# Kernel tuning notes

Measured on AMD Instinct MI355X. Metric: run time of the kernel, lower is better.

Reference implementation:

```python
import jax, jax.numpy as jnp
import numpy as np

HEADS = 4
DIM_HEAD = 128
DIM = 512
FMAP = 32
BATCH = 16


def setup_inputs() -> dict:
    key = jax.random.key(0)
    k1, k2, k3, k4 = jax.random.split(key, 4)
    inner = HEADS * DIM_HEAD
    scale = DIM_HEAD ** -0.5
    fmap = jax.random.normal(k1, (BATCH, DIM, FMAP, FMAP), dtype=jnp.float32)
    # 1x1 conv weight, squeezed: [3*inner_dim, dim]
    w_qkv = jax.random.normal(k2, (3 * inner, DIM), dtype=jnp.float32) * (DIM ** -0.5)
    emb_h = jax.random.normal(k3, (FMAP, DIM_HEAD), dtype=jnp.float32) * scale
    emb_w = jax.random.normal(k4, (FMAP, DIM_HEAD), dtype=jnp.float32) * scale
    return {"fmap": fmap, "w_qkv": w_qkv, "emb_h": emb_h, "emb_w": emb_w}


def reference(fmap, w_qkv, emb_h, emb_w):
    b, c, h, w = fmap.shape
    n = h * w
    scale = DIM_HEAD ** -0.5
    # 1x1 conv == channel matmul: [b, 3*inner, h, w]
    qkv = jnp.einsum('bchw,oc->bohw', fmap, w_qkv)
    # split and rearrange 'b (hd d) x y -> b hd (x y) d'
    qkv = qkv.reshape(b, 3, HEADS, DIM_HEAD, n)          # b 3 H d n
    qkv = jnp.transpose(qkv, (1, 0, 2, 4, 3))            # 3 b H n d
    q, k, v = qkv[0], qkv[1], qkv[2]
    q = q * scale
    # content logits
    sim = jnp.einsum('bhid,bhjd->bhij', q, k)
    # absolute position bias: emb[(x,y)] = emb_h[x] + emb_w[y]
    emb = (emb_h[:, None, :] + emb_w[None, :, :]).reshape(n, DIM_HEAD)
    sim = sim + jnp.einsum('bhid,jd->bhij', q, emb)
    attn = jax.nn.softmax(sim, axis=-1)
    out = jnp.einsum('bhij,bhjd->bhid', attn, v)         # b H n d
    # 'b h (x y) d -> b (h d) x y'
    out = jnp.transpose(out, (0, 1, 3, 2)).reshape(b, HEADS * DIM_HEAD, h, w)
    return out
```

## Files before the change

kernel.cpp:

```cpp
#include <hip/hip_runtime.h>

#define HEADS 4
#define DHEAD 128
#define DIM   512
#define NTOK  1024
#define BATCH 16
#define OCH   1536

typedef unsigned short u16;
typedef short bf16x8 __attribute__((ext_vector_type(8)));
typedef float f32x4  __attribute__((ext_vector_type(4)));

struct alignas(8) us4 { u16 x, y, z, w; };

static __device__ __forceinline__ u16 f2bf(float f) {
    unsigned int u = __float_as_uint(f);
    u = (u + 0x7FFFu + ((u >> 16) & 1u)) >> 16;
    return (u16)u;
}
static __device__ __forceinline__ float bf2f(u16 h) {
    return __uint_as_float(((unsigned int)h) << 16);
}

__global__ __launch_bounds__(256)
void prep_ft(const float* __restrict__ F, u16* __restrict__ fthi, u16* __restrict__ ftlo)
{
    __shared__ float T[32][33];
    const int n0 = blockIdx.x * 32;
    const int c0 = blockIdx.y * 32;
    const int b  = blockIdx.z;
    const int tid = threadIdx.x;

    {
        const int c  = tid >> 3;
        const int n4 = (tid & 7) * 4;
        const float4 f4 = *(const float4*)(&F[((size_t)b * DIM + c0 + c) * NTOK + n0 + n4]);
        T[c][n4 + 0] = f4.x; T[c][n4 + 1] = f4.y; T[c][n4 + 2] = f4.z; T[c][n4 + 3] = f4.w;
    }
    __syncthreads();
    {
        const int n  = tid >> 3;
        const int c4 = (tid & 7) * 4;
        us4 H, L;
        float v0 = T[c4 + 0][n], v1 = T[c4 + 1][n], v2 = T[c4 + 2][n], v3 = T[c4 + 3][n];
        H.x = f2bf(v0); L.x = f2bf(v0 - bf2f(H.x));
        H.y = f2bf(v1); L.y = f2bf(v1 - bf2f(H.y));
        H.z = f2bf(v2); L.z = f2bf(v2 - bf2f(H.z));
        H.w = f2bf(v3); L.w = f2bf(v3 - bf2f(H.w));
        const size_t o = ((size_t)b * NTOK + n0 + n) * DIM + c0 + c4;
        *(us4*)&fthi[o] = H;
        *(us4*)&ftlo[o] = L;
    }
}

__global__ __launch_bounds__(256)
void prep_w(const float* __restrict__ W, u16* __restrict__ wbhi, u16* __restrict__ wblo)
{
    const size_t idx = ((size_t)blockIdx.x * 256 + threadIdx.x) * 8;
    const float4 a = *(const float4*)(&W[idx]);
    const float4 b = *(const float4*)(&W[idx + 4]);
    float v[8] = {a.x, a.y, a.z, a.w, b.x, b.y, b.z, b.w};
    u16 H[8], L[8];
#pragma unroll
    for (int j = 0; j < 8; ++j) {
        H[j] = f2bf(v[j]);
        L[j] = f2bf(v[j] - bf2f(H[j]));
    }
    *(bf16x8*)&wbhi[idx] = *(bf16x8*)H;
    *(bf16x8*)&wblo[idx] = *(bf16x8*)L;
}

__global__ __launch_bounds__(256)
void qkv_mfma(const u16* __restrict__ fthi, const u16* __restrict__ ftlo,
              const u16* __restrict__ wbhi, const u16* __restrict__ wblo,
              const float* __restrict__ EH, const float* __restrict__ EW,
              u16* __restrict__ qhi, u16* __restrict__ qlo,
              u16* __restrict__ khi, u16* __restrict__ klo,
              u16* __restrict__ vtg)
{
    __shared__ u16 smem[16384];
    u16* Ah = smem;
    u16* Al = smem + 4096;
    u16* Bh = smem + 8192;
    u16* Bl = smem + 12288;
    float* Od = (float*)smem;

    const int tid  = threadIdx.x;
    const int lane = tid & 63;
    const int wave = tid >> 6;
    const int l15  = lane & 15;
    const int lg   = lane >> 4;
    const int wm   = wave >> 1;
    const int wn   = wave & 1;

    const int ii = blockIdx.x * 64;
    const int oo = blockIdx.y * 64;
    const int b  = blockIdx.z;
    const size_t fbase = (size_t)b * NTOK * DIM;

    f32x4 acc[2][2];
#pragma unroll
    for (int mf = 0; mf < 2; ++mf)
#pragma unroll
        for (int nf = 0; nf < 2; ++nf) { acc[mf][nf][0] = 0.f; acc[mf][nf][1] = 0.f; acc[mf][nf][2] = 0.f; acc[mf][nf][3] = 0.f; }

    for (int kt = 0; kt < DIM; kt += 64) {
        __syncthreads();
#pragma unroll
        for (int u = 0; u < 2; ++u) {
            const int idx = tid + 256 * u;
            const int j  = idx >> 3;
            const int dc = (idx & 7) * 8;
            const int ld = j * 64 + (dc ^ ((j & 7) << 3));
            const size_t ga = fbase + (size_t)(ii + j) * DIM + kt + dc;
            const size_t gb = (size_t)(oo + j) * DIM + kt + dc;
            *(bf16x8*)&Ah[ld] = *(const bf16x8*)(fthi + ga);
            *(bf16x8*)&Al[ld] = *(const bf16x8*)(ftlo + ga);
            *(bf16x8*)&Bh[ld] = *(const bf16x8*)(wbhi + gb);
            *(bf16x8*)&Bl[ld] = *(const bf16x8*)(wblo + gb);
        }
        __syncthreads();

#pragma unroll
        for (int kc = 0; kc < 2; ++kc) {
            const int ko = kc * 32 + lg * 8;
            bf16x8 af_h[2], af_l[2], bf_h[2], bf_l[2];
#pragma unroll
            for (int mf = 0; mf < 2; ++mf) {
                const int ar = wm * 32 + mf * 16 + l15;
                const int off = ar * 64 + (ko ^ ((ar & 7) << 3));
                af_h[mf] = *(const bf16x8*)&Ah[off];
                af_l[mf] = *(const bf16x8*)&Al[off];
            }
#pragma unroll
            for (int nf = 0; nf < 2; ++nf) {
                const int br = wn * 32 + nf * 16 + l15;
                const int off = br * 64 + (ko ^ ((br & 7) << 3));
                bf_h[nf] = *(const bf16x8*)&Bh[off];
                bf_l[nf] = *(const bf16x8*)&Bl[off];
            }
#pragma unroll
            for (int mf = 0; mf < 2; ++mf)
#pragma unroll
                for (int nf = 0; nf < 2; ++nf) {
                    acc[mf][nf] = __builtin_amdgcn_mfma_f32_16x16x32_bf16(af_h[mf], bf_h[nf], acc[mf][nf], 0, 0, 0);
                    acc[mf][nf] = __builtin_amdgcn_mfma_f32_16x16x32_bf16(af_h[mf], bf_l[nf], acc[mf][nf], 0, 0, 0);
                    acc[mf][nf] = __builtin_amdgcn_mfma_f32_16x16x32_bf16(af_l[mf], bf_h[nf], acc[mf][nf], 0, 0, 0);
                }
        }
    }

    __syncthreads();
#pragma unroll
    for (int mf = 0; mf < 2; ++mf)
#pragma unroll
        for (int nf = 0; nf < 2; ++nf)
#pragma unroll
            for (int r = 0; r < 4; ++r)
                Od[(wm * 32 + mf * 16 + lg * 4 + r) * 68 + wn * 32 + nf * 16 + l15] = acc[mf][nf][r];
    __syncthreads();

    const int s  = oo >> 9;
    const int h  = (oo >> 7) & 3;
    const int d0 = oo & 127;
    const int bh = b * HEADS + h;
    const float scale = 0.08838834764831845f;

    if (s == 2) {
#pragma unroll
        for (int u = 0; u < 2; ++u) {
            const int idx = tid + 256 * u;
            const int dr = idx >> 3;
            const int tc = (idx & 7) * 8;
            u16 P[8];
#pragma unroll
            for (int j = 0; j < 8; ++j)
                P[j] = f2bf(Od[(tc + j) * 68 + dr]);
            *(bf16x8*)&vtg[((size_t)bh * DHEAD + d0 + dr) * NTOK + ii + tc] = *(bf16x8*)P;
        }
    } else {
        u16* hi = s ? khi : qhi;
        u16* lo = s ? klo : qlo;
#pragma unroll
        for (int u = 0; u < 2; ++u) {
            const int idx = tid + 256 * u;
            const int tr = idx >> 3;
            const int dc = (idx & 7) * 8;
            const int i  = ii + tr;
            float v[8];
            const float4 p0 = *(const float4*)&Od[tr * 68 + dc];
            const float4 p1 = *(const float4*)&Od[tr * 68 + dc + 4];
            v[0] = p0.x; v[1] = p0.y; v[2] = p0.z; v[3] = p0.w;
            v[4] = p1.x; v[5] = p1.y; v[6] = p1.z; v[7] = p1.w;
            if (s == 0) {
#pragma unroll
                for (int j = 0; j < 8; ++j) v[j] *= scale;
            } else {
                const float* eh = &EH[(i >> 5) * DHEAD + d0 + dc];
                const float* ew = &EW[(i & 31) * DHEAD + d0 + dc];
                const float4 e0 = *(const float4*)eh, e1 = *(const float4*)(eh + 4);
                const float4 w0 = *(const float4*)ew, w1 = *(const float4*)(ew + 4);
                v[0] += e0.x + w0.x; v[1] += e0.y + w0.y; v[2] += e0.z + w0.z; v[3] += e0.w + w0.w;
                v[4] += e1.x + w1.x; v[5] += e1.y + w1.y; v[6] += e1.z + w1.z; v[7] += e1.w + w1.w;
            }
            u16 H[8], L[8];
#pragma unroll
            for (int j = 0; j < 8; ++j) {
                H[j] = f2bf(v[j]);
                L[j] = f2bf(v[j] - bf2f(H[j]));
            }
            const size_t o = ((size_t)bh * NTOK + i) * DHEAD + d0 + dc;
            *(bf16x8*)&hi[o] = *(bf16x8*)H;
            *(bf16x8*)&lo[o] = *(bf16x8*)L;
        }
    }
}

#define QB 64
#define KB 64

__global__ __launch_bounds__(256, 2)
void attn_mfma(const u16* __restrict__ qh, const u16* __restrict__ ql,
               const u16* __restrict__ kh, const u16* __restrict__ kl,
               const u16* __restrict__ vtg, float* __restrict__ out)
{
    __shared__ u16 smem[28672];
    u16* Kh = smem;
    u16* Kl = smem + 8192;
    u16* Vt = smem + 16384;
    u16* Pl = smem + 24576;
    float* Od = (float*)smem;

    const int tid  = threadIdx.x;
    const int lane = tid & 63;
    const int wave = tid >> 6;
    const int l15  = lane & 15;
    const int lg   = lane >> 4;

    const int ii = blockIdx.x * QB;
    const int bh = blockIdx.y;
    const size_t base = (size_t)bh * NTOK * DHEAD;

    bf16x8 qfh[4], qfl[4];
    {
        const size_t qoff = base + (size_t)(ii + wave * 16 + l15) * DHEAD + lg * 8;
#pragma unroll
        for (int kc = 0; kc < 4; ++kc) {
            qfh[kc] = *(const bf16x8*)(qh + qoff + kc * 32);
            qfl[kc] = *(const bf16x8*)(ql + qoff + kc * 32);
        }
    }

    f32x4 o[8];
#pragma unroll
    for (int n = 0; n < 8; ++n) { o[n][0] = 0.f; o[n][1] = 0.f; o[n][2] = 0.f; o[n][3] = 0.f; }
    float mrow[4], lrow[4];
#pragma unroll
    for (int r = 0; r < 4; ++r) { mrow[r] = -3.0e38f; lrow[r] = 0.f; }

    for (int jt = 0; jt < NTOK / KB; ++jt) {
        __syncthreads();
#pragma unroll
        for (int u = 0; u < 4; ++u) {
            const int idx = tid + 256 * u;
            const int j  = idx >> 4;
            const int dc = (idx & 15) * 8;
            const size_t g = base + (size_t)(jt * KB + j) * DHEAD + dc;
            const int ld = j * DHEAD + (dc ^ ((j & 7) << 3));
            *(bf16x8*)&Kh[ld] = *(const bf16x8*)(kh + g);
            *(bf16x8*)&Kl[ld] = *(const bf16x8*)(kl + g);
        }
#pragma unroll
        for (int u = 0; u < 4; ++u) {
            const int idx = tid + 256 * u;
            const int d  = idx >> 3;
            const int jc = (idx & 7) * 8;
            const size_t g = base + (size_t)d * NTOK + jt * KB + jc;
            *(bf16x8*)&Vt[d * KB + (jc ^ ((d & 7) << 3))] = *(const bf16x8*)(vtg + g);
        }
        __syncthreads();

        f32x4 s[4];
#pragma unroll
        for (int n = 0; n < 4; ++n) {
            f32x4 acc = {0.f, 0.f, 0.f, 0.f};
            const int j  = n * 16 + l15;
            const int ro = j * DHEAD;
            const int sw = (j & 7) << 3;
#pragma unroll
            for (int kc = 0; kc < 4; ++kc) {
                const int off = ro + ((kc * 32 + lg * 8) ^ sw);
                const bf16x8 kb = *(const bf16x8*)&Kh[off];
                const bf16x8 lb = *(const bf16x8*)&Kl[off];
                acc = __builtin_amdgcn_mfma_f32_16x16x32_bf16(qfh[kc], kb, acc, 0, 0, 0);
                acc = __builtin_amdgcn_mfma_f32_16x16x32_bf16(qfh[kc], lb, acc, 0, 0, 0);
                acc = __builtin_amdgcn_mfma_f32_16x16x32_bf16(qfl[kc], kb, acc, 0, 0, 0);
            }
            s[n] = acc;
        }

        float tmax[4];
#pragma unroll
        for (int r = 0; r < 4; ++r)
            tmax[r] = fmaxf(fmaxf(s[0][r], s[1][r]), fmaxf(s[2][r], s[3][r]));
#pragma unroll
        for (int off = 1; off < 16; off <<= 1)
#pragma unroll
            for (int r = 0; r < 4; ++r)
                tmax[r] = fmaxf(tmax[r], __shfl_xor(tmax[r], off));

        float fr[4], psum[4];
#pragma unroll
        for (int r = 0; r < 4; ++r) {
            const float mn = fmaxf(mrow[r], tmax[r]);
            fr[r] = __expf(mrow[r] - mn);
            mrow[r] = mn;
            psum[r] = 0.f;
        }
        const int pbase = wave * 1024;
#pragma unroll
        for (int n = 0; n < 4; ++n)
#pragma unroll
            for (int r = 0; r < 4; ++r) {
                const float p = __expf(s[n][r] - mrow[r]);
                psum[r] += p;
                const int row = lg * 4 + r;
                Pl[pbase + row * KB + ((n * 16 + l15) ^ ((row & 7) << 3))] = f2bf(p);
            }
#pragma unroll
        for (int off = 1; off < 16; off <<= 1)
#pragma unroll
            for (int r = 0; r < 4; ++r)
                psum[r] += __shfl_xor(psum[r], off);
#pragma unroll
        for (int r = 0; r < 4; ++r) lrow[r] = lrow[r] * fr[r] + psum[r];
#pragma unroll
        for (int n = 0; n < 8; ++n)
#pragma unroll
            for (int r = 0; r < 4; ++r) o[n][r] *= fr[r];

        const bf16x8 pf0 = *(const bf16x8*)&Pl[pbase + l15 * KB + ((lg * 8) ^ ((l15 & 7) << 3))];
        const bf16x8 pf1 = *(const bf16x8*)&Pl[pbase + l15 * KB + ((32 + lg * 8) ^ ((l15 & 7) << 3))];
#pragma unroll
        for (int nd = 0; nd < 8; ++nd) {
            const int d  = nd * 16 + l15;
            const int vo = d * KB;
            const int sw = (d & 7) << 3;
            o[nd] = __builtin_amdgcn_mfma_f32_16x16x32_bf16(
                        pf0, *(const bf16x8*)&Vt[vo + ((lg * 8) ^ sw)], o[nd], 0, 0, 0);
            o[nd] = __builtin_amdgcn_mfma_f32_16x16x32_bf16(
                        pf1, *(const bf16x8*)&Vt[vo + ((32 + lg * 8) ^ sw)], o[nd], 0, 0, 0);
        }
    }

    __syncthreads();
    float invl[4];
#pragma unroll
    for (int r = 0; r < 4; ++r) invl[r] = 1.0f / lrow[r];
#pragma unroll
    for (int nd = 0; nd < 8; ++nd)
#pragma unroll
        for (int r = 0; r < 4; ++r)
            Od[(nd * 16 + l15) * 72 + wave * 16 + lg * 4 + r] = o[nd][r] * invl[r];
    __syncthreads();

    const int b = bh >> 2, h = bh & 3;
    float* dst = out + ((size_t)b * 512 + h * DHEAD) * NTOK + ii;
#pragma unroll
    for (int u = 0; u < 4; ++u) {
        const int idx = tid + 256 * u;
        const int d  = idx >> 3;
        const int jc = (idx & 7) * 8;
        *(float4*)(dst + (size_t)d * NTOK + jc)     = *(const float4*)&Od[d * 72 + jc];
        *(float4*)(dst + (size_t)d * NTOK + jc + 4) = *(const float4*)&Od[d * 72 + jc + 4];
    }
}

extern "C" void kernel_launch(void* const* d_in, const int* in_sizes, int n_in,
                              void* d_out, int out_size, void* d_ws, size_t ws_size,
                              hipStream_t stream)
{
    (void)in_sizes; (void)n_in; (void)out_size; (void)ws_size;
    const float* fmap  = (const float*)d_in[0];
    const float* w_qkv = (const float*)d_in[1];
    const float* eh    = (const float*)d_in[2];
    const float* ew    = (const float*)d_in[3];
    float* out = (float*)d_out;

    const size_t per = (size_t)BATCH * HEADS * NTOK * DHEAD;
    u16* qhi  = (u16*)d_ws;
    u16* qlo  = qhi + per;
    u16* khi  = qlo + per;
    u16* klo  = khi + per;
    u16* vtg  = klo + per;
    u16* fthi = vtg + per;
    u16* ftlo = fthi + per;
    u16* wbhi = ftlo + per;
    u16* wblo = wbhi + (size_t)OCH * DIM;

    hipLaunchKernelGGL(prep_ft, dim3(NTOK / 32, DIM / 32, BATCH), dim3(256), 0, stream,
                       fmap, fthi, ftlo);
    hipLaunchKernelGGL(prep_w, dim3((OCH * DIM) / (256 * 8)), dim3(256), 0, stream,
                       w_qkv, wbhi, wblo);
    hipLaunchKernelGGL(qkv_mfma, dim3(NTOK / 64, OCH / 64, BATCH), dim3(256), 0, stream,
                       fthi, ftlo, wbhi, wblo, eh, ew, qhi, qlo, khi, klo, vtg);
    hipLaunchKernelGGL(attn_mfma, dim3(NTOK / QB, BATCH * HEADS), dim3(256), 0, stream,
                       qhi, qlo, khi, klo, vtg, out);
}
```

Baseline: 307.3 us.

## Prefetch next K/V and GEMM tiles into registers during MFMA compute

In both the QKV projection GEMM and the attention kernel, the global loads for the next tile are issued into registers before the current tile's MFMA work and written to shared memory after it. This hides global memory latency behind compute without adding a second LDS buffer. The attention kernel also raises wave priority around its MFMA sections with s_setprio, and the QKV kernel gains a min-2-blocks launch bound. The cost is more live registers per thread, which can cut occupancy or cause spills.

Result: no change. 301.4 us (-1.9%).

```diff
diff --git a/kernel.cpp b/kernel.cpp
--- a/kernel.cpp
+++ b/kernel.cpp
@@ -70,7 +70,7 @@
     *(bf16x8*)&wblo[idx] = *(bf16x8*)L;
 }
 
-__global__ __launch_bounds__(256)
+__global__ __launch_bounds__(256, 2)
 void qkv_mfma(const u16* __restrict__ fthi, const u16* __restrict__ ftlo,
               const u16* __restrict__ wbhi, const u16* __restrict__ wblo,
               const float* __restrict__ EH, const float* __restrict__ EW,
@@ -98,28 +98,45 @@
     const int b  = blockIdx.z;
     const size_t fbase = (size_t)b * NTOK * DIM;
 
+    const int jrow = tid >> 3;
+    const int dc   = (tid & 7) * 8;
+    const int ld0  = jrow * 64 + (dc ^ ((jrow & 7) << 3));
+    const size_t ga0 = fbase + (size_t)(ii + jrow) * DIM + dc;
+    const size_t gb0 = (size_t)(oo + jrow) * DIM + dc;
+
     f32x4 acc[2][2];
 #pragma unroll
     for (int mf = 0; mf < 2; ++mf)
 #pragma unroll
         for (int nf = 0; nf < 2; ++nf) { acc[mf][nf][0] = 0.f; acc[mf][nf][1] = 0.f; acc[mf][nf][2] = 0.f; acc[mf][nf][3] = 0.f; }
 
+    bf16x8 pah[2], pal[2], pbh[2], pbl[2];
+#pragma unroll
+    for (int u = 0; u < 2; ++u) {
+        pah[u] = *(const bf16x8*)(fthi + ga0 + (size_t)u * 32 * DIM);
+        pal[u] = *(const bf16x8*)(ftlo + ga0 + (size_t)u * 32 * DIM);
+        pbh[u] = *(const bf16x8*)(wbhi + gb0 + (size_t)u * 32 * DIM);
+        pbl[u] = *(const bf16x8*)(wblo + gb0 + (size_t)u * 32 * DIM);
+    }
+#pragma unroll
+    for (int u = 0; u < 2; ++u) {
+        *(bf16x8*)&Ah[ld0 + 2048 * u] = pah[u];
+        *(bf16x8*)&Al[ld0 + 2048 * u] = pal[u];
+        *(bf16x8*)&Bh[ld0 + 2048 * u] = pbh[u];
+        *(bf16x8*)&Bl[ld0 + 2048 * u] = pbl[u];
+    }
+    __syncthreads();
+
     for (int kt = 0; kt < DIM; kt += 64) {
-        __syncthreads();
-#pragma unroll
-        for (int u = 0; u < 2; ++u) {
-            const int idx = tid + 256 * u;
-            const int j  = idx >> 3;
-            const int dc = (idx & 7) * 8;
-            const int ld = j * 64 + (dc ^ ((j & 7) << 3));
-            const size_t ga = fbase + (size_t)(ii + j) * DIM + kt + dc;
-            const size_t gb = (size_t)(oo + j) * DIM + kt + dc;
-            *(bf16x8*)&Ah[ld] = *(const bf16x8*)(fthi + ga);
-            *(bf16x8*)&Al[ld] = *(const bf16x8*)(ftlo + ga);
-            *(bf16x8*)&Bh[ld] = *(const bf16x8*)(wbhi + gb);
-            *(bf16x8*)&Bl[ld] = *(const bf16x8*)(wblo + gb);
-        }
-        __syncthreads();
+        if (kt < DIM - 64) {
+#pragma unroll
+            for (int u = 0; u < 2; ++u) {
+                pah[u] = *(const bf16x8*)(fthi + ga0 + kt + 64 + (size_t)u * 32 * DIM);
+                pal[u] = *(const bf16x8*)(ftlo + ga0 + kt + 64 + (size_t)u * 32 * DIM);
+                pbh[u] = *(const bf16x8*)(wbhi + gb0 + kt + 64 + (size_t)u * 32 * DIM);
+                pbl[u] = *(const bf16x8*)(wblo + gb0 + kt + 64 + (size_t)u * 32 * DIM);
+            }
+        }
 
 #pragma unroll
         for (int kc = 0; kc < 2; ++kc) {
@@ -148,9 +165,19 @@
                     acc[mf][nf] = __builtin_amdgcn_mfma_f32_16x16x32_bf16(af_l[mf], bf_h[nf], acc[mf][nf], 0, 0, 0);
                 }
         }
-    }
-
-    __syncthreads();
+        __syncthreads();
+        if (kt < DIM - 64) {
+#pragma unroll
+            for (int u = 0; u < 2; ++u) {
+                *(bf16x8*)&Ah[ld0 + 2048 * u] = pah[u];
+                *(bf16x8*)&Al[ld0 + 2048 * u] = pal[u];
+                *(bf16x8*)&Bh[ld0 + 2048 * u] = pbh[u];
+                *(bf16x8*)&Bl[ld0 + 2048 * u] = pbl[u];
+            }
+        }
+        __syncthreads();
+    }
+
 #pragma unroll
     for (int mf = 0; mf < 2; ++mf)
 #pragma unroll
@@ -185,19 +212,19 @@
         for (int u = 0; u < 2; ++u) {
             const int idx = tid + 256 * u;
             const int tr = idx >> 3;
-            const int dc = (idx & 7) * 8;
+            const int dcc = (idx & 7) * 8;
             const int i  = ii + tr;
             float v[8];
-            const float4 p0 = *(const float4*)&Od[tr * 68 + dc];
-            const float4 p1 = *(const float4*)&Od[tr * 68 + dc + 4];
+            const float4 p0 = *(const float4*)&Od[tr * 68 + dcc];
+            const float4 p1 = *(const float4*)&Od[tr * 68 + dcc + 4];
             v[0] = p0.x; v[1] = p0.y; v[2] = p0.z; v[3] = p0.w;
             v[4] = p1.x; v[5] = p1.y; v[6] = p1.z; v[7] = p1.w;
             if (s == 0) {
 #pragma unroll
                 for (int j = 0; j < 8; ++j) v[j] *= scale;
             } else {
-                const float* eh = &EH[(i >> 5) * DHEAD + d0 + dc];
-                const float* ew = &EW[(i & 31) * DHEAD + d0 + dc];
+                const float* eh = &EH[(i >> 5) * DHEAD + d0 + dcc];
+                const float* ew = &EW[(i & 31) * DHEAD + d0 + dcc];
                 const float4 e0 = *(const float4*)eh, e1 = *(const float4*)(eh + 4);
                 const float4 w0 = *(const float4*)ew, w1 = *(const float4*)(ew + 4);
                 v[0] += e0.x + w0.x; v[1] += e0.y + w0.y; v[2] += e0.z + w0.z; v[3] += e0.w + w0.w;
@@ -209,7 +236,7 @@
                 H[j] = f2bf(v[j]);
                 L[j] = f2bf(v[j] - bf2f(H[j]));
             }
-            const size_t o = ((size_t)bh * NTOK + i) * DHEAD + d0 + dc;
+            const size_t o = ((size_t)bh * NTOK + i) * DHEAD + d0 + dcc;
             *(bf16x8*)&hi[o] = *(bf16x8*)H;
             *(bf16x8*)&lo[o] = *(bf16x8*)L;
         }
@@ -241,6 +268,15 @@
     const int bh = blockIdx.y;
     const size_t base = (size_t)bh * NTOK * DHEAD;
 
+    const int kj  = tid >> 4;
+    const int kdc = (tid & 15) * 8;
+    const int vd  = tid >> 3;
+    const int vjc = (tid & 7) * 8;
+    const int ldk0 = kj * DHEAD + (kdc ^ ((kj & 7) << 3));
+    const int ldv0 = vd * KB   + (vjc ^ ((vd & 7) << 3));
+    const size_t gk0 = base + (size_t)kj * DHEAD + kdc;
+    const size_t gv0 = base + (size_t)vd * NTOK + vjc;
+
     bf16x8 qfh[4], qfl[4];
     {
         const size_t qoff = base + (size_t)(ii + wave * 16 + l15) * DHEAD + lg * 8;
@@ -258,29 +294,35 @@
 #pragma unroll
     for (int r = 0; r < 4; ++r) { mrow[r] = -3.0e38f; lrow[r] = 0.f; }
 
+    bf16x8 pkh[4], pkl[4], pv[4];
+#pragma unroll
+    for (int u = 0; u < 4; ++u) {
+        pkh[u] = *(const bf16x8*)(kh  + gk0 + 2048 * u);
+        pkl[u] = *(const bf16x8*)(kl  + gk0 + 2048 * u);
+        pv[u]  = *(const bf16x8*)(vtg + gv0 + 32768 * (size_t)u);
+    }
+#pragma unroll
+    for (int u = 0; u < 4; ++u) {
+        *(bf16x8*)&Kh[ldk0 + 2048 * u] = pkh[u];
+        *(bf16x8*)&Kl[ldk0 + 2048 * u] = pkl[u];
+        *(bf16x8*)&Vt[ldv0 + 2048 * u] = pv[u];
+    }
+    __syncthreads();
+
     for (int jt = 0; jt < NTOK / KB; ++jt) {
-        __syncthreads();
-#pragma unroll
-        for (int u = 0; u < 4; ++u) {
-            const int idx = tid + 256 * u;
-            const int j  = idx >> 4;
-            const int dc = (idx & 15) * 8;
-            const size_t g = base + (size_t)(jt * KB + j) * DHEAD + dc;
-            const int ld = j * DHEAD + (dc ^ ((j & 7) << 3));
-            *(bf16x8*)&Kh[ld] = *(const bf16x8*)(kh + g);
-            *(bf16x8*)&Kl[ld] = *(const bf16x8*)(kl + g);
-        }
-#pragma unroll
-        for (int u = 0; u < 4; ++u) {
-            const int idx = tid + 256 * u;
-            const int d  = idx >> 3;
-            const int jc = (idx & 7) * 8;
-            const size_t g = base + (size_t)d * NTOK + jt * KB + jc;
-            *(bf16x8*)&Vt[d * KB + (jc ^ ((d & 7) << 3))] = *(const bf16x8*)(vtg + g);
-        }
-        __syncthreads();
+        if (jt < NTOK / KB - 1) {
+            const size_t gk = gk0 + (size_t)(jt + 1) * 8192;
+            const size_t gv = gv0 + (size_t)(jt + 1) * 64;
+#pragma unroll
+            for (int u = 0; u < 4; ++u) {
+                pkh[u] = *(const bf16x8*)(kh  + gk + 2048 * u);
+                pkl[u] = *(const bf16x8*)(kl  + gk + 2048 * u);
+                pv[u]  = *(const bf16x8*)(vtg + gv + 32768 * (size_t)u);
+            }
+        }
 
         f32x4 s[4];
+        __builtin_amdgcn_s_setprio(1);
 #pragma unroll
         for (int n = 0; n < 4; ++n) {
             f32x4 acc = {0.f, 0.f, 0.f, 0.f};
@@ -298,6 +340,7 @@
             }
             s[n] = acc;
         }
+        __builtin_amdgcn_s_setprio(0);
 
         float tmax[4];
 #pragma unroll
@@ -341,6 +384,7 @@
 
         const bf16x8 pf0 = *(const bf16x8*)&Pl[pbase + l15 * KB + ((lg * 8) ^ ((l15 & 7) << 3))];
         const bf16x8 pf1 = *(const bf16x8*)&Pl[pbase + l15 * KB + ((32 + lg * 8) ^ ((l15 & 7) << 3))];
+        __builtin_amdgcn_s_setprio(1);
 #pragma unroll
         for (int nd = 0; nd < 8; ++nd) {
             const int d  = nd * 16 + l15;
@@ -351,6 +395,18 @@
             o[nd] = __builtin_amdgcn_mfma_f32_16x16x32_bf16(
                         pf1, *(const bf16x8*)&Vt[vo + ((32 + lg * 8) ^ sw)], o[nd], 0, 0, 0);
         }
+        __builtin_amdgcn_s_setprio(0);
+
+        __syncthreads();
+        if (jt < NTOK / KB - 1) {
+#pragma unroll
+            for (int u = 0; u < 4; ++u) {
+                *(bf16x8*)&Kh[ldk0 + 2048 * u] = pkh[u];
+                *(bf16x8*)&Kl[ldk0 + 2048 * u] = pkl[u];
+                *(bf16x8*)&Vt[ldv0 + 2048 * u] = pv[u];
+            }
+        }
+        __syncthreads();
     }
 
     __syncthreads();
```
